# Optimization experiments

Hardware: AMD Instinct MI355X
Metric: run time of the kernel (lower is better)

## Reference

```python
import jax, jax.numpy as jnp
import numpy as np

D = 256       # state dim (x.shape[-1], size of jnp.eye in f)
H = 1024      # vf hidden width (4*D)
B = 8         # batch of prior samples (outer vmap over keys)
N_STEPS = 8   # fixed Dopri5 steps over t in [0, 1]
DT = 1.0 / N_STEPS

# Dopri5 Butcher tableau (b7 = 0, so 6 effective stages for a fixed step)
C = [0.0, 1.0/5.0, 3.0/10.0, 4.0/5.0, 8.0/9.0, 1.0]
A = [
    [],
    [1.0/5.0],
    [3.0/40.0, 9.0/40.0],
    [44.0/45.0, -56.0/15.0, 32.0/9.0],
    [19372.0/6561.0, -25360.0/2187.0, 64448.0/6561.0, -212.0/729.0],
    [9017.0/3168.0, -355.0/33.0, 46732.0/5247.0, 49.0/176.0, -5103.0/18656.0],
]
BW = [35.0/384.0, 0.0, 500.0/1113.0, 125.0/192.0, -2187.0/6784.0, 11.0/84.0]


def setup_inputs() -> dict:
    key = jax.random.key(0)
    ks = jax.random.split(key, 5)
    s1 = 1.0 / np.sqrt(D)
    s2 = 1.0 / np.sqrt(H)
    return {
        "x0": jax.random.normal(ks[0], (B, D), dtype=jnp.float32),
        "W1": jax.random.normal(ks[1], (D, H), dtype=jnp.float32) * s1,
        "b1": jnp.zeros((H,), dtype=jnp.float32),
        "wt": jax.random.normal(ks[2], (H,), dtype=jnp.float32) * 0.1,
        "W2": jax.random.normal(ks[3], (H, D), dtype=jnp.float32) * s2,
        "b2": jnp.zeros((D,), dtype=jnp.float32),
        "mu": jax.random.normal(ks[4], (D,), dtype=jnp.float32),
    }


def reference(x0, W1, b1, wt, W2, b2, mu):
    tmap = jax.tree_util.tree_map

    def vf(t, x):  # x: [D] -> [D], time-conditioned tanh MLP
        h = jnp.tanh(x @ W1 + b1 + wt * t)
        return h @ W2 + b2

    def logp(x):  # target (unnormalized) Gaussian log-density
        return -0.5 * jnp.sum((x - mu) ** 2)

    gradlogp = jax.grad(logp)
    eye = jnp.eye(D, dtype=x0.dtype)

    def dyn_single(t, x):  # augmented CNF dynamics for one sample
        f = lambda y: vf(t, y)
        # vmap(jvp) over basis vectors -> full Jacobian (rows here = J^T rows)
        primal, jac = jax.vmap(lambda v: jax.jvp(f, (x,), (v,)))(eye)
        dxdt = primal[0]                      # [D]
        dlogq = -jnp.trace(jac)               # -tr(J) (transpose-invariant)
        dkl = -jnp.vdot(gradlogp(x), dxdt)
        dvfn = jnp.sum(dxdt ** 2)
        djfn = jnp.sum(jac ** 2)              # Frobenius norm^2 of J
        return dxdt, dlogq, dkl, dvfn, djfn

    def dyn(t, state):
        x = state[0]  # [B, D]
        return jax.vmap(lambda xi: dyn_single(t, xi))(x)

    def rk_step(y, t):  # one fixed Dopri5 step on the pytree state
        ks = []
        for i in range(6):
            if i == 0:
                yi = y
            else:
                coefs = A[i]
                yi = tmap(
                    lambda yy, *kk: yy + DT * sum(a * k for a, k in zip(coefs, kk)),
                    y, *ks)
            ks.append(dyn(t + C[i] * DT, yi))
        y_next = tmap(
            lambda yy, *kk: yy + DT * sum(b * k for b, k in zip(BW, kk)),
            y, *ks)
        return y_next, None

    # standard-normal prior log-density at x0
    log_q0 = -0.5 * (D * jnp.log(2.0 * jnp.pi) + jnp.sum(x0 ** 2, axis=-1))
    zeros = jnp.zeros((B,), dtype=x0.dtype)
    y0 = (x0, log_q0, zeros, zeros, zeros)
    ts = jnp.arange(N_STEPS, dtype=x0.dtype) * DT
    yT, _ = jax.lax.scan(rk_step, y0, ts)
    z, log_q1, kl, vfn, jfn = yT
    # pack outputs: [B, D+4] = [z | log_q1 | kl | total_vf_norm | total_jac_frob_norm]
    return jnp.concatenate(
        [z, log_q1[:, None], kl[:, None], vfn[:, None], jfn[:, None]], axis=1)
```

## Files before the change

kernel.cpp:

```cpp
#include <hip/hip_runtime.h>
#include <math.h>

#define Hn 1024
#define Dn 256
#define Bn 8
#define DTf 0.125f

typedef __attribute__((ext_vector_type(4))) float f32x4;

constexpr float kA[6][5] = {
  {0.f, 0.f, 0.f, 0.f, 0.f},
  {1.0f/5.0f, 0.f, 0.f, 0.f, 0.f},
  {3.0f/40.0f, 9.0f/40.0f, 0.f, 0.f, 0.f},
  {44.0f/45.0f, -56.0f/15.0f, 32.0f/9.0f, 0.f, 0.f},
  {19372.0f/6561.0f, -25360.0f/2187.0f, 64448.0f/6561.0f, -212.0f/729.0f, 0.f},
  {9017.0f/3168.0f, -355.0f/33.0f, 46732.0f/5247.0f, 49.0f/176.0f, -5103.0f/18656.0f}
};
constexpr float kC[6] = {0.f, 0.2f, 0.3f, 0.8f, 8.0f/9.0f, 1.0f};
constexpr float kBW[6] = {35.0f/384.0f, 0.f, 500.0f/1113.0f, 125.0f/192.0f,
                          -2187.0f/6784.0f, 11.0f/84.0f};

__device__ __forceinline__ float fast_tanh(float x) {
  const float ax = fabsf(x);
  const float z = __expf(-2.0f * ax);
  const float t = (1.0f - z) * __builtin_amdgcn_rcpf(1.0f + z);
  return copysignf(t, x);
}

__global__ __launch_bounds__(256) void precomp(
    const float* __restrict__ W1, const float* __restrict__ W2,
    const float* __restrict__ b2, const float* __restrict__ x0,
    float* __restrict__ Mm, float* __restrict__ Zz, float* __restrict__ cc,
    float* __restrict__ bz, float* __restrict__ ux, float* __restrict__ hbuf,
    float* __restrict__ scal, unsigned* __restrict__ flags) {
  __shared__ float sm[8704];
  const int tid = threadIdx.x;
  const int wg = blockIdx.x;
  if (wg < 256) {
    float* a1k  = sm;
    float* a1l  = sm + 2048;
    float* w2kT = sm + 4096;
    float* w2lT = sm + 6400;
    const int k0 = (wg & 15) * 64, l0 = (wg >> 4) * 64;
    const int kq = tid & 15, lq = tid >> 4;
    float g1[4][4] = {}, g2[4][4] = {};
    for (int dc = 0; dc < 8; dc++) {
      const int d0 = dc * 32;
      __syncthreads();
      for (int idx = tid; idx < 2048; idx += 256) {
        const int r1 = idx >> 6, c1 = idx & 63;
        a1k[r1 * 64 + c1] = W1[(d0 + r1) * Hn + k0 + c1];
        a1l[r1 * 64 + c1] = W1[(d0 + r1) * Hn + l0 + c1];
      }
      for (int idx = tid; idx < 2048; idx += 256) {
        const int r1 = idx >> 5, c1 = idx & 31;
        w2kT[c1 * 72 + r1] = W2[(k0 + r1) * Dn + d0 + c1];
        w2lT[c1 * 72 + r1] = W2[(l0 + r1) * Dn + d0 + c1];
      }
      __syncthreads();
      #pragma unroll 4
      for (int dd = 0; dd < 32; dd++) {
        const float4 ak = *(const float4*)&a1k[dd * 64 + kq * 4];
        const float4 al = *(const float4*)&a1l[dd * 64 + lq * 4];
        const float4 wk = *(const float4*)&w2kT[dd * 72 + kq * 4];
        const float4 wl = *(const float4*)&w2lT[dd * 72 + lq * 4];
        const float akv[4] = {ak.x, ak.y, ak.z, ak.w};
        const float alv[4] = {al.x, al.y, al.z, al.w};
        const float wkv[4] = {wk.x, wk.y, wk.z, wk.w};
        const float wlv[4] = {wl.x, wl.y, wl.z, wl.w};
        #pragma unroll
        for (int i = 0; i < 4; i++)
          #pragma unroll
          for (int j = 0; j < 4; j++) {
            g1[i][j] += akv[i] * alv[j];
            g2[i][j] += wkv[i] * wlv[j];
          }
      }
    }
    #pragma unroll
    for (int i = 0; i < 4; i++)
      #pragma unroll
      for (int j = 0; j < 4; j++)
        Mm[(k0 + kq * 4 + i) * Hn + l0 + lq * 4 + j] = g1[i][j] * g2[i][j];
  } else if (wg < 512) {
    float* w2lT = sm;
    float* w1t  = sm + 4608;
    const int bw = wg - 256;
    const int e0 = (bw & 15) * 64, l0 = (bw >> 4) * 64;
    const int eq = tid & 15, lq = tid >> 4;
    float acc[4][4] = {};
    for (int dc = 0; dc < 4; dc++) {
      const int d0 = dc * 64;
      __syncthreads();
      for (int idx = tid; idx < 4096; idx += 256) {
        const int r1 = idx >> 6, c1 = idx & 63;
        w2lT[c1 * 72 + r1] = W2[(l0 + r1) * Dn + d0 + c1];
        w1t[r1 * 64 + c1] = W1[(d0 + r1) * Hn + e0 + c1];
      }
      __syncthreads();
      #pragma unroll 4
      for (int dd = 0; dd < 64; dd++) {
        const float4 wv = *(const float4*)&w2lT[dd * 72 + lq * 4];
        const float4 xv = *(const float4*)&w1t[dd * 64 + eq * 4];
        const float wvv[4] = {wv.x, wv.y, wv.z, wv.w};
        const float xvv[4] = {xv.x, xv.y, xv.z, xv.w};
        #pragma unroll
        for (int i = 0; i < 4; i++)
          #pragma unroll
          for (int j = 0; j < 4; j++)
            acc[i][j] += wvv[i] * xvv[j];
      }
    }
    #pragma unroll
    for (int i = 0; i < 4; i++)
      #pragma unroll
      for (int j = 0; j < 4; j++)
        Zz[(l0 + lq * 4 + i) * Hn + e0 + eq * 4 + j] = acc[i][j];
  } else if (wg == 512) {
    if (tid < 64) scal[tid] = 0.f;
    if (tid == 0) flags[1024] = 0u;
  } else if (wg < 517) {
    const int k = (wg - 513) * 256 + tid;
    float s = 0.f;
    for (int d = 0; d < Dn; d++) s += W1[d * Hn + k] * W2[k * Dn + d];
    cc[k] = s;
  } else if (wg < 521) {
    const int e = (wg - 517) * 256 + tid;
    float s = 0.f;
    for (int d = 0; d < Dn; d++) s += b2[d] * W1[d * Hn + e];
    bz[e] = s;
  } else if (wg < 553) {
    const int idx = (wg - 521) * 256 + tid;
    const int b = idx >> 10, e = idx & 1023;
    float s = 0.f;
    for (int d = 0; d < Dn; d++) s += x0[b * Dn + d] * W1[d * Hn + e];
    ux[b * Hn + e] = s;
  } else {
    float* base = hbuf + (size_t)(wg - 553) * 8192;
    const f32x4 sent = {2.0f, 2.0f, 2.0f, 2.0f};
    for (int idx = tid; idx < 2048; idx += 256)
      *(f32x4*)&base[idx * 4] = sent;
  }
}

__global__ __launch_bounds__(512) void ode_main(
    const float* __restrict__ x0, const float* __restrict__ b1,
    const float* __restrict__ wt, const float* __restrict__ W2g,
    const float* __restrict__ b2, const float* __restrict__ mu,
    float* __restrict__ out,
    const float* __restrict__ Mm, const float* __restrict__ Zz,
    const float* __restrict__ cc, const float* __restrict__ bz,
    const float* __restrict__ ux, float* __restrict__ hbuf,
    float* __restrict__ scal, unsigned* __restrict__ flags) {
  __shared__ float Ms[16 * 1028];
  __shared__ float hsf[2][8 * 1028];
  __shared__ float red[2][8][8][20];

  const int tid = threadIdx.x;
  const int wg = blockIdx.x;
  int role, cidx;
  if (wg < 64) { role = 0; cidx = wg; }
  else if (wg < 128) { role = 1; cidx = wg - 64; }
  else { role = 2; cidx = wg - 128; }
  const int wv = tid >> 6, lane = tid & 63;
  const int cp = lane & 7, ks = lane >> 3;
  const int b = tid >> 4, cl = tid & 15;
  const int lh = lane >> 5, lc = lane & 31;

  float ubr = 0.f, xbr = 0.f;
  float b1c = 0.f, wtc = 0.f, bzc = 0.f, ccr = 0.f, b2c = 0.f, muc = 0.f;
  float gkr[6] = {}, kr[6] = {};
  float acc_a = 0.f, acc_b = 0.f;

  if (role == 0) {
    if (tid < 128) {
      const int col = 16 * cidx + cl;
      b1c = b1[col]; wtc = wt[col]; bzc = bz[col];
      ubr = ux[b * Hn + col];
      const float h0 = fast_tanh(ubr + b1c);
      __hip_atomic_store(&hbuf[b * 1024 + col], h0, __ATOMIC_RELAXED,
                         __HIP_MEMORY_SCOPE_AGENT);
    }
  } else if (role == 1) {
    if (tid < 128) ccr = cc[16 * cidx + cl];
  } else {
    if (tid < 128) {
      const int d = 16 * cidx + cl;
      xbr = x0[b * Dn + d];
      muc = mu[d]; b2c = b2[d];
      float v = xbr * xbr;
      v += __shfl_xor(v, 1, 64); v += __shfl_xor(v, 2, 64);
      v += __shfl_xor(v, 4, 64); v += __shfl_xor(v, 8, 64);
      if (cl == 0) atomicAdd(&scal[b * 8 + 4], v);
    }
  }

  {
    const float* msrc = (role == 0) ? Zz : (role == 1) ? Mm : W2g;
    const int mld = (role == 2) ? Dn : Hn;
    const int cb = 16 * cidx;
    for (int j = 0; j < 32; ++j) {
      const int idx = j * 512 + tid;
      const int l = idx >> 4, c = idx & 15;
      Ms[c * 1028 + l] = msrc[l * mld + cb + c];
    }
  }
  __syncthreads();

  int ep = 0;
  for (int n = 0; n < 8; ++n) {
    #pragma unroll
    for (int i = 0; i < 6; ++i) {
      const int s = n * 6 + i;
      if (role == 0 && s == 47) break;
      if (role == 1 && i == 1) continue;

      const float* hb0 = hbuf + (size_t)s * 8192 + (size_t)lh * 1024 +
                         128 * wv + 4 * lc;
      const float* q0 = hb0;
      const float* q1 = hb0 + 2048;
      const float* q2 = hb0 + 4096;
      const float* q3 = hb0 + 6144;
      f32x4 v0, v1, v2, v3;
      {
        int miss = 0;
        while (true) {
          asm volatile(
              "global_load_dwordx4 %0, %1, off sc0 sc1\n\t"
              "s_waitcnt vmcnt(0)"
              : "=&v"(v3) : "v"(q3) : "memory");
          const int bad3 = (v3.x == 2.0f) | (v3.y == 2.0f) |
                           (v3.z == 2.0f) | (v3.w == 2.0f);
          if (!__any(bad3)) break;
          if (role == 0) {
            if (miss > 2)       __builtin_amdgcn_s_sleep(4);
            else if (miss == 2) __builtin_amdgcn_s_sleep(2);
            else if (miss == 1) __builtin_amdgcn_s_sleep(1);
          } else {
            if (miss > 0) __builtin_amdgcn_s_sleep(32);
            else          __builtin_amdgcn_s_sleep(8);
          }
          ++miss;
        }
        while (true) {
          asm volatile(
              "global_load_dwordx4 %0, %4, off sc0 sc1\n\t"
              "global_load_dwordx4 %1, %5, off sc0 sc1\n\t"
              "global_load_dwordx4 %2, %6, off sc0 sc1\n\t"
              "global_load_dwordx4 %3, %7, off sc0 sc1\n\t"
              "s_waitcnt vmcnt(0)"
              : "=&v"(v0), "=&v"(v1), "=&v"(v2), "=&v"(v3)
              : "v"(q0), "v"(q1), "v"(q2), "v"(q3)
              : "memory");
          const int bad =
              (v0.x == 2.0f) | (v0.y == 2.0f) | (v0.z == 2.0f) | (v0.w == 2.0f) |
              (v1.x == 2.0f) | (v1.y == 2.0f) | (v1.z == 2.0f) | (v1.w == 2.0f) |
              (v2.x == 2.0f) | (v2.y == 2.0f) | (v2.z == 2.0f) | (v2.w == 2.0f) |
              (v3.x == 2.0f) | (v3.y == 2.0f) | (v3.z == 2.0f) | (v3.w == 2.0f);
          if (!__any(bad)) break;
          __builtin_amdgcn_s_sleep(1);
        }
      }
      if (role == 1) {
        v0 = 1.0f - v0 * v0; v1 = 1.0f - v1 * v1;
        v2 = 1.0f - v2 * v2; v3 = 1.0f - v3 * v3;
      }
      {
        const int kofs = 128 * wv + 4 * lc;
        *(f32x4*)&hsf[ep][(0 + lh) * 1028 + kofs] = v0;
        *(f32x4*)&hsf[ep][(2 + lh) * 1028 + kofs] = v1;
        *(f32x4*)&hsf[ep][(4 + lh) * 1028 + kofs] = v2;
        *(f32x4*)&hsf[ep][(6 + lh) * 1028 + kofs] = v3;
      }

      float av[16] = {};
      #pragma unroll
      for (int j = 0; j < 4; ++j) {
        const int kb = 128 * wv + 4 * ks + 32 * j;
        const f32x4 z0 = *(const f32x4*)&Ms[(2 * cp) * 1028 + kb];
        const f32x4 z1 = *(const f32x4*)&Ms[(2 * cp + 1) * 1028 + kb];
        #pragma unroll
        for (int bb = 0; bb < 8; ++bb) {
          const f32x4 hb = *(const f32x4*)&hsf[ep][bb * 1028 + kb];
          av[bb]     += z0.x * hb.x + z0.y * hb.y + z0.z * hb.z + z0.w * hb.w;
          av[8 + bb] += z1.x * hb.x + z1.y * hb.y + z1.z * hb.z + z1.w * hb.w;
        }
      }
      #pragma unroll
      for (int q = 0; q < 16; ++q) {
        av[q] += __shfl_xor(av[q], 8, 64);
        av[q] += __shfl_xor(av[q], 16, 64);
        av[q] += __shfl_xor(av[q], 32, 64);
      }
      if (ks == 0) {
        float* rp = &red[ep][wv][cp][0];
        #pragma unroll
        for (int q = 0; q < 16; ++q) rp[q] = av[q];
      }
      __syncthreads();

      if (tid < 128) {
        float r = 0.f;
        #pragma unroll
        for (int w = 0; w < 8; ++w)
          r += red[ep][w][cl >> 1][(cl & 1) * 8 + b];
        if (role == 0) {
          gkr[i] = r + bzc;
          float u;
          if (i == 5) {
            ubr += DTf * (kBW[0] * gkr[0] + kBW[2] * gkr[2] + kBW[3] * gkr[3] +
                          kBW[4] * gkr[4] + kBW[5] * gkr[5]);
            u = ubr + b1c + wtc * ((float)(n + 1) * DTf);
          } else {
            u = ubr + b1c + wtc * (((float)n + kC[i + 1]) * DTf);
            #pragma unroll
            for (int j2 = 0; j2 <= i; ++j2) u += DTf * kA[i + 1][j2] * gkr[j2];
          }
          const float hn2 = fast_tanh(u);
          __hip_atomic_store(
              &hbuf[(size_t)(s + 1) * 8192 + b * 1024 + 16 * cidx + cl], hn2,
              __ATOMIC_RELAXED, __HIP_MEMORY_SCOPE_AGENT);
        } else if (role == 1) {
          const float sv = hsf[ep][b * 1028 + 16 * cidx + cl];
          float u1 = sv * r;
          float u2 = sv * ccr;
          u1 += __shfl_xor(u1, 1, 64); u2 += __shfl_xor(u2, 1, 64);
          u1 += __shfl_xor(u1, 2, 64); u2 += __shfl_xor(u2, 2, 64);
          u1 += __shfl_xor(u1, 4, 64); u2 += __shfl_xor(u2, 4, 64);
          u1 += __shfl_xor(u1, 8, 64); u2 += __shfl_xor(u2, 8, 64);
          if (cl == 0) {
            const float wgt = DTf * kBW[i];
            acc_a += -wgt * u2;
            acc_b += wgt * u1;
          }
        } else {
          const float kv = r + b2c;
          kr[i] = kv;
          float xi = xbr;
          #pragma unroll
          for (int j2 = 0; j2 < i; ++j2) xi += DTf * kA[i][j2] * kr[j2];
          float u1 = (xi - muc) * kv;
          float u2 = kv * kv;
          u1 += __shfl_xor(u1, 1, 64); u2 += __shfl_xor(u2, 1, 64);
          u1 += __shfl_xor(u1, 2, 64); u2 += __shfl_xor(u2, 2, 64);
          u1 += __shfl_xor(u1, 4, 64); u2 += __shfl_xor(u2, 4, 64);
          u1 += __shfl_xor(u1, 8, 64); u2 += __shfl_xor(u2, 8, 64);
          if (cl == 0) {
            const float wgt = DTf * kBW[i];
            acc_a += wgt * u1;
            acc_b += wgt * u2;
          }
          if (i == 5)
            xbr += DTf * (kBW[0] * kr[0] + kBW[2] * kr[2] + kBW[3] * kr[3] +
                          kBW[4] * kr[4] + kBW[5] * kr[5]);
        }
      }
      ep ^= 1;
    }
  }

  if (role == 1) {
    if (tid < 128 && cl == 0) {
      atomicAdd(&scal[b * 8 + 0], acc_a);
      atomicAdd(&scal[b * 8 + 3], acc_b);
    }
  } else if (role == 2) {
    if (tid < 128) out[b * 260 + 16 * cidx + cl] = xbr;
    if (tid < 128 && cl == 0) {
      atomicAdd(&scal[b * 8 + 1], acc_a);
      atomicAdd(&scal[b * 8 + 2], acc_b);
    }
  }
  if (role != 0) {
    asm volatile("s_waitcnt vmcnt(0)" ::: "memory");
    __syncthreads();
    if (tid == 0) {
      const unsigned old = __hip_atomic_fetch_add(&flags[1024], 1u,
                                                  __ATOMIC_RELAXED,
                                                  __HIP_MEMORY_SCOPE_AGENT);
      if (old == 79u) {
        for (int bb = 0; bb < Bn; ++bb) {
          const float trj = __hip_atomic_load(&scal[bb * 8 + 0], __ATOMIC_RELAXED, __HIP_MEMORY_SCOPE_AGENT);
          const float kl  = __hip_atomic_load(&scal[bb * 8 + 1], __ATOMIC_RELAXED, __HIP_MEMORY_SCOPE_AGENT);
          const float vfn = __hip_atomic_load(&scal[bb * 8 + 2], __ATOMIC_RELAXED, __HIP_MEMORY_SCOPE_AGENT);
          const float jfn = __hip_atomic_load(&scal[bb * 8 + 3], __ATOMIC_RELAXED, __HIP_MEMORY_SCOPE_AGENT);
          const float xsq = __hip_atomic_load(&scal[bb * 8 + 4], __ATOMIC_RELAXED, __HIP_MEMORY_SCOPE_AGENT);
          out[bb * 260 + 256] = -0.5f * (470.49652900079245f + xsq) + trj;
          out[bb * 260 + 257] = kl;
          out[bb * 260 + 258] = vfn;
          out[bb * 260 + 259] = jfn;
        }
      }
    }
  }
}

extern "C" void kernel_launch(void* const* d_in, const int* in_sizes, int n_in,
                              void* d_out, int out_size, void* d_ws, size_t ws_size,
                              hipStream_t stream) {
  (void)in_sizes; (void)n_in; (void)out_size; (void)ws_size;
  const float* x0 = (const float*)d_in[0];
  const float* W1 = (const float*)d_in[1];
  const float* b1 = (const float*)d_in[2];
  const float* wt = (const float*)d_in[3];
  const float* W2 = (const float*)d_in[4];
  const float* b2 = (const float*)d_in[5];
  const float* mu = (const float*)d_in[6];
  float* out = (float*)d_out;
  float* w = (float*)d_ws;

  float* Mm   = w;
  float* Zz   = Mm + 1048576;
  float* cc   = Zz + 1048576;
  float* bz   = cc + 1024;
  float* ux   = bz + 1024;
  float* hbuf = ux + 8192;
  float* scal = hbuf + 393216;
  unsigned* flags = (unsigned*)(scal + 64);

  precomp<<<dim3(601), dim3(256), 0, stream>>>(W1, W2, b2, x0, Mm, Zz, cc, bz,
                                               ux, hbuf, scal, flags);
  ode_main<<<dim3(144), dim3(512), 0, stream>>>(x0, b1, wt, W2, b2, mu, out,
                                                Mm, Zz, cc, bz, ux, hbuf, scal,
                                                flags);
}
```

Measured before the change: 250.3 us.

## Move small precomputes into ode_main and precompute stage inputs before spin-wait

Removes the cc, bz and ux precompute blocks from the first kernel and computes them inside ode_main's role prologues, shrinking the precomp grid. The partial stage argument (all terms except the newest k) is now computed before the spin-wait on hbuf, shortening the critical path after the data arrives. Role 0 also polls all four vectors at once with shorter sleeps, and the other roles use a fixed sleep. The cost is serial 256-length dot products per thread at ode_main start and heavier polling traffic.

```diff
diff --git a/kernel.cpp b/kernel.cpp
--- a/kernel.cpp
+++ b/kernel.cpp
@@ -29,10 +29,9 @@
 
 __global__ __launch_bounds__(256) void precomp(
     const float* __restrict__ W1, const float* __restrict__ W2,
-    const float* __restrict__ b2, const float* __restrict__ x0,
-    float* __restrict__ Mm, float* __restrict__ Zz, float* __restrict__ cc,
-    float* __restrict__ bz, float* __restrict__ ux, float* __restrict__ hbuf,
-    float* __restrict__ scal, unsigned* __restrict__ flags) {
+    float* __restrict__ Mm, float* __restrict__ Zz,
+    float* __restrict__ hbuf, float* __restrict__ scal,
+    unsigned* __restrict__ flags) {
   __shared__ float sm[8704];
   const int tid = threadIdx.x;
   const int wg = blockIdx.x;
@@ -118,25 +117,9 @@
         Zz[(l0 + lq * 4 + i) * Hn + e0 + eq * 4 + j] = acc[i][j];
   } else if (wg == 512) {
     if (tid < 64) scal[tid] = 0.f;
-    if (tid == 0) flags[1024] = 0u;
-  } else if (wg < 517) {
-    const int k = (wg - 513) * 256 + tid;
-    float s = 0.f;
-    for (int d = 0; d < Dn; d++) s += W1[d * Hn + k] * W2[k * Dn + d];
-    cc[k] = s;
-  } else if (wg < 521) {
-    const int e = (wg - 517) * 256 + tid;
-    float s = 0.f;
-    for (int d = 0; d < Dn; d++) s += b2[d] * W1[d * Hn + e];
-    bz[e] = s;
-  } else if (wg < 553) {
-    const int idx = (wg - 521) * 256 + tid;
-    const int b = idx >> 10, e = idx & 1023;
-    float s = 0.f;
-    for (int d = 0; d < Dn; d++) s += x0[b * Dn + d] * W1[d * Hn + e];
-    ux[b * Hn + e] = s;
+    if (tid == 0) flags[0] = 0u;
   } else {
-    float* base = hbuf + (size_t)(wg - 553) * 8192;
+    float* base = hbuf + (size_t)(wg - 513) * 8192;
     const f32x4 sent = {2.0f, 2.0f, 2.0f, 2.0f};
     for (int idx = tid; idx < 2048; idx += 256)
       *(f32x4*)&base[idx * 4] = sent;
@@ -144,14 +127,13 @@
 }
 
 __global__ __launch_bounds__(512) void ode_main(
-    const float* __restrict__ x0, const float* __restrict__ b1,
-    const float* __restrict__ wt, const float* __restrict__ W2g,
-    const float* __restrict__ b2, const float* __restrict__ mu,
-    float* __restrict__ out,
+    const float* __restrict__ x0, const float* __restrict__ W1,
+    const float* __restrict__ b1, const float* __restrict__ wt,
+    const float* __restrict__ W2g, const float* __restrict__ b2,
+    const float* __restrict__ mu, float* __restrict__ out,
     const float* __restrict__ Mm, const float* __restrict__ Zz,
-    const float* __restrict__ cc, const float* __restrict__ bz,
-    const float* __restrict__ ux, float* __restrict__ hbuf,
-    float* __restrict__ scal, unsigned* __restrict__ flags) {
+    float* __restrict__ hbuf, float* __restrict__ scal,
+    unsigned* __restrict__ flags) {
   __shared__ float Ms[16 * 1028];
   __shared__ float hsf[2][8 * 1028];
   __shared__ float red[2][8][8][20];
@@ -175,14 +157,26 @@
   if (role == 0) {
     if (tid < 128) {
       const int col = 16 * cidx + cl;
-      b1c = b1[col]; wtc = wt[col]; bzc = bz[col];
-      ubr = ux[b * Hn + col];
+      b1c = b1[col]; wtc = wt[col];
+      float ub = 0.f, bzv = 0.f;
+      for (int d = 0; d < Dn; ++d) {
+        const float w1v = W1[d * Hn + col];
+        ub  += x0[b * Dn + d] * w1v;
+        bzv += b2[d] * w1v;
+      }
+      ubr = ub; bzc = bzv;
       const float h0 = fast_tanh(ubr + b1c);
       __hip_atomic_store(&hbuf[b * 1024 + col], h0, __ATOMIC_RELAXED,
                          __HIP_MEMORY_SCOPE_AGENT);
     }
   } else if (role == 1) {
-    if (tid < 128) ccr = cc[16 * cidx + cl];
+    if (tid < 128) {
+      const int col = 16 * cidx + cl;
+      float cv = 0.f;
+      for (int d = 0; d < Dn; ++d)
+        cv += W1[d * Hn + col] * W2g[col * Dn + d];
+      ccr = cv;
+    }
   } else {
     if (tid < 128) {
       const int d = 16 * cidx + cl;
@@ -215,6 +209,18 @@
       if (role == 0 && s == 47) break;
       if (role == 1 && i == 1) continue;
 
+      float upre = 0.f;
+      if (role == 0 && tid < 128) {
+        if (i == 5) {
+          upre = ubr + DTf * (kBW[0] * gkr[0] + kBW[2] * gkr[2] +
+                              kBW[3] * gkr[3] + kBW[4] * gkr[4]);
+        } else {
+          upre = ubr + b1c + wtc * (((float)n + kC[i + 1]) * DTf);
+          #pragma unroll
+          for (int j2 = 0; j2 < i; ++j2) upre += DTf * kA[i + 1][j2] * gkr[j2];
+        }
+      }
+
       const float* hb0 = hbuf + (size_t)s * 8192 + (size_t)lh * 1024 +
                          128 * wv + 4 * lc;
       const float* q0 = hb0;
@@ -222,8 +228,29 @@
       const float* q2 = hb0 + 4096;
       const float* q3 = hb0 + 6144;
       f32x4 v0, v1, v2, v3;
-      {
+      if (role == 0) {
         int miss = 0;
+        while (true) {
+          asm volatile(
+              "global_load_dwordx4 %0, %4, off sc0 sc1\n\t"
+              "global_load_dwordx4 %1, %5, off sc0 sc1\n\t"
+              "global_load_dwordx4 %2, %6, off sc0 sc1\n\t"
+              "global_load_dwordx4 %3, %7, off sc0 sc1\n\t"
+              "s_waitcnt vmcnt(0)"
+              : "=&v"(v0), "=&v"(v1), "=&v"(v2), "=&v"(v3)
+              : "v"(q0), "v"(q1), "v"(q2), "v"(q3)
+              : "memory");
+          const int bad =
+              (v0.x == 2.0f) | (v0.y == 2.0f) | (v0.z == 2.0f) | (v0.w == 2.0f) |
+              (v1.x == 2.0f) | (v1.y == 2.0f) | (v1.z == 2.0f) | (v1.w == 2.0f) |
+              (v2.x == 2.0f) | (v2.y == 2.0f) | (v2.z == 2.0f) | (v2.w == 2.0f) |
+              (v3.x == 2.0f) | (v3.y == 2.0f) | (v3.z == 2.0f) | (v3.w == 2.0f);
+          if (!__any(bad)) break;
+          if (miss >= 3)      __builtin_amdgcn_s_sleep(2);
+          else if (miss == 2) __builtin_amdgcn_s_sleep(1);
+          ++miss;
+        }
+      } else {
         while (true) {
           asm volatile(
               "global_load_dwordx4 %0, %1, off sc0 sc1\n\t"
@@ -232,15 +259,7 @@
           const int bad3 = (v3.x == 2.0f) | (v3.y == 2.0f) |
                            (v3.z == 2.0f) | (v3.w == 2.0f);
           if (!__any(bad3)) break;
-          if (role == 0) {
-            if (miss > 2)       __builtin_amdgcn_s_sleep(4);
-            else if (miss == 2) __builtin_amdgcn_s_sleep(2);
-            else if (miss == 1) __builtin_amdgcn_s_sleep(1);
-          } else {
-            if (miss > 0) __builtin_amdgcn_s_sleep(32);
-            else          __builtin_amdgcn_s_sleep(8);
-          }
-          ++miss;
+          __builtin_amdgcn_s_sleep(16);
         }
         while (true) {
           asm volatile(
@@ -308,13 +327,10 @@
           gkr[i] = r + bzc;
           float u;
           if (i == 5) {
-            ubr += DTf * (kBW[0] * gkr[0] + kBW[2] * gkr[2] + kBW[3] * gkr[3] +
-                          kBW[4] * gkr[4] + kBW[5] * gkr[5]);
+            ubr = upre + DTf * kBW[5] * gkr[5];
             u = ubr + b1c + wtc * ((float)(n + 1) * DTf);
           } else {
-            u = ubr + b1c + wtc * (((float)n + kC[i + 1]) * DTf);
-            #pragma unroll
-            for (int j2 = 0; j2 <= i; ++j2) u += DTf * kA[i + 1][j2] * gkr[j2];
+            u = upre + DTf * kA[i + 1][i] * gkr[i];
           }
           const float hn2 = fast_tanh(u);
           __hip_atomic_store(
@@ -375,7 +391,7 @@
     asm volatile("s_waitcnt vmcnt(0)" ::: "memory");
     __syncthreads();
     if (tid == 0) {
-      const unsigned old = __hip_atomic_fetch_add(&flags[1024], 1u,
+      const unsigned old = __hip_atomic_fetch_add(&flags[0], 1u,
                                                   __ATOMIC_RELAXED,
                                                   __HIP_MEMORY_SCOPE_AGENT);
       if (old == 79u) {
@@ -411,16 +427,11 @@
 
   float* Mm   = w;
   float* Zz   = Mm + 1048576;
-  float* cc   = Zz + 1048576;
-  float* bz   = cc + 1024;
-  float* ux   = bz + 1024;
-  float* hbuf = ux + 8192;
+  float* hbuf = Zz + 1048576;
   float* scal = hbuf + 393216;
   unsigned* flags = (unsigned*)(scal + 64);
 
-  precomp<<<dim3(601), dim3(256), 0, stream>>>(W1, W2, b2, x0, Mm, Zz, cc, bz,
-                                               ux, hbuf, scal, flags);
-  ode_main<<<dim3(144), dim3(512), 0, stream>>>(x0, b1, wt, W2, b2, mu, out,
-                                                Mm, Zz, cc, bz, ux, hbuf, scal,
-                                                flags);
+  precomp<<<dim3(561), dim3(256), 0, stream>>>(W1, W2, Mm, Zz, hbuf, scal, flags);
+  ode_main<<<dim3(144), dim3(512), 0, stream>>>(x0, W1, b1, wt, W2, b2, mu, out,
+                                                Mm, Zz, hbuf, scal, flags);
 }
```

Result: slower. 272.8 us (+9.0%).
